# Kernel tuning notes

Hardware: AMD Instinct MI355X
Metric: run time of the kernel (lower is better)

Reference implementation:

```python
import jax, jax.numpy as jnp
import numpy as np

N_NODES = 50000
N_EDGES = 600000
D = 128


def _clip(x, c=1.0):
    # per-row L2 clip: x / max(||x|| / c, 1)
    n = jnp.linalg.norm(x, axis=-1, keepdims=True)
    return x / jnp.maximum(n / c, 1.0)


def _priv_sage_conv(x, edge_index, W, b, noise):
    # PrivSAGEConv.forward with perturbation_mode='aggr', root_weight=False
    xc = _clip(x, c=1.0)
    src, dst = edge_index[0], edge_index[1]
    # propagate: gather messages from source nodes, scatter-add at targets
    msg = jax.ops.segment_sum(xc[src], dst, num_segments=x.shape[0])  # [N, D]
    agg = xc + msg + noise  # self term + neighbor sum + DP noise
    return agg @ W.T + b


def setup_inputs() -> dict:
    key = jax.random.key(0)
    ks = jax.random.split(key, 8)
    x = jax.random.normal(ks[0], (N_NODES, D), dtype=jnp.float32)
    edge_index = jax.random.randint(ks[1], (2, N_EDGES), 0, N_NODES, dtype=jnp.int64)
    scale = 1.0 / np.sqrt(D)
    W1 = jax.random.normal(ks[2], (D, D), dtype=jnp.float32) * scale
    b1 = jnp.zeros((D,), dtype=jnp.float32)
    W2 = jax.random.normal(ks[3], (D, D), dtype=jnp.float32) * scale
    b2 = jnp.zeros((D,), dtype=jnp.float32)
    noise1 = jax.random.normal(ks[4], (N_NODES, D), dtype=jnp.float32)
    noise2 = jax.random.normal(ks[5], (N_NODES, D), dtype=jnp.float32)
    return {"x": x, "edge_index": edge_index, "W1": W1, "b1": b1,
            "W2": W2, "b2": b2, "noise1": noise1, "noise2": noise2}


def reference(x, edge_index, W1, b1, W2, b2, noise1, noise2):
    # Layer 1: conv -> (no batchnorm) -> dropout(identity, eval) -> SELU -> stack-combine
    h = _priv_sage_conv(x, edge_index, W1, b1, noise1)
    h = jax.nn.selu(h)
    # Layer 2: last layer, is_pred_module=True -> raw output
    out = _priv_sage_conv(h, edge_index, W2, b2, noise2)
    return out
```

## Files before the change

kernel.cpp:

```cpp
#include <hip/hip_runtime.h>

#define NN 50000
#define NE 600000
#define DD 128
#define NPAD 50048
#define SCAN_BLOCKS 49

typedef __attribute__((ext_vector_type(8))) short bf16x8;
typedef __attribute__((ext_vector_type(4))) float f32x4;

__device__ __forceinline__ float bf2f(unsigned int u16) {
    union { unsigned int i; float f; } v; v.i = u16 << 16; return v.f;
}
__device__ __forceinline__ unsigned short f2bf(float f) {
    union { float f; unsigned int i; } v; v.f = f;
    unsigned int i = v.i + 0x7FFFu + ((v.i >> 16) & 1u);
    return (unsigned short)(i >> 16);
}
__device__ __forceinline__ float wred64(float v) {
    #pragma unroll
    for (int o = 32; o; o >>= 1) v += __shfl_xor(v, o, 64);
    return v;
}
__device__ __forceinline__ int tame16(unsigned int u) {
    int e = (int)((u >> 7) & 0xFF);
    return (e >= 100 && e <= 133) ? 1 : 0;
}

__global__ void probe_k(const int* __restrict__ ei,
                        const unsigned int* __restrict__ xw,
                        const unsigned int* __restrict__ w1w,
                        const unsigned int* __restrict__ nzw,
                        int* __restrict__ flags) {
    const int lane = threadIdx.x;
    int nz = 0;
    #pragma unroll
    for (int i = 0; i < 4; ++i) nz |= ei[2 * (lane * 4 + i) + 1];
    int tx = tame16(xw[lane] & 0xFFFFu);
    int tw = tame16(w1w[lane] & 0xFFFFu);
    int tn = tame16(nzw[lane] & 0xFFFFu);
    #pragma unroll
    for (int o = 32; o; o >>= 1) {
        nz |= __shfl_xor(nz, o, 64);
        tx += __shfl_xor(tx, o, 64);
        tw += __shfl_xor(tw, o, 64);
        tn += __shfl_xor(tn, o, 64);
    }
    if (lane == 0) {
        flags[0] = (nz == 0) ? 1 : 0;
        flags[1] = (tx >= 48) ? 1 : 0;
        flags[2] = (tw >= 48) ? 1 : 0;
        flags[3] = (tn >= 48) ? 1 : 0;
    }
}

__global__ __launch_bounds__(256) void convert_k(
    const void* __restrict__ W1, const void* __restrict__ b1,
    const void* __restrict__ W2, const void* __restrict__ b2,
    const int* __restrict__ flags,
    unsigned short* __restrict__ W1b, unsigned short* __restrict__ b1b,
    unsigned short* __restrict__ W2b, unsigned short* __restrict__ b2b) {
    const int i = blockIdx.x * blockDim.x + threadIdx.x;
    if (i >= DD * DD) return;
    if (flags[2]) {
        W1b[i] = ((const unsigned short*)W1)[i];
        W2b[i] = ((const unsigned short*)W2)[i];
        if (i < DD) { b1b[i] = ((const unsigned short*)b1)[i];
                      b2b[i] = ((const unsigned short*)b2)[i]; }
    } else {
        W1b[i] = f2bf(((const float*)W1)[i]);
        W2b[i] = f2bf(((const float*)W2)[i]);
        if (i < DD) { b1b[i] = f2bf(((const float*)b1)[i]);
                      b2b[i] = f2bf(((const float*)b2)[i]); }
    }
}

__global__ __launch_bounds__(256) void hist_k(
    const int* __restrict__ ei, const int* __restrict__ flags,
    int* __restrict__ deg) {
    const int e = blockIdx.x * blockDim.x + threadIdx.x;
    if (e >= NE) return;
    const int d = flags[0] ? (int)((const long long*)ei)[NE + e] : ei[NE + e];
    atomicAdd(&deg[d], 1);
}

__global__ __launch_bounds__(1024) void scan1_k(
    const int* __restrict__ deg, int* __restrict__ offs,
    int* __restrict__ bsum) {
    __shared__ int wsum[16];
    __shared__ int wbase[16];
    __shared__ int tot_s;
    const int tid = threadIdx.x, lane = tid & 63, wv = tid >> 6;
    const int i = blockIdx.x * 1024 + tid;
    const int v = (i < NN) ? deg[i] : 0;
    int incl = v;
    #pragma unroll
    for (int off = 1; off < 64; off <<= 1) {
        int t = __shfl_up(incl, off, 64);
        if (lane >= off) incl += t;
    }
    if (lane == 63) wsum[wv] = incl;
    __syncthreads();
    if (wv == 0 && lane < 16) {
        const int wv_v = wsum[lane];
        int wincl = wv_v;
        #pragma unroll
        for (int off = 1; off < 16; off <<= 1) {
            int t = __shfl_up(wincl, off, 64);
            if (lane >= off) wincl += t;
        }
        wbase[lane] = wincl - wv_v;
        if (lane == 15) tot_s = wincl;
    }
    __syncthreads();
    if (i < NN) offs[i] = wbase[wv] + incl - v;
    if (tid == 0) bsum[blockIdx.x] = tot_s;
}

__global__ __launch_bounds__(1024) void scan2_k(
    int* __restrict__ offs, int* __restrict__ cursor,
    const int* __restrict__ bsum) {
    __shared__ int base_s;
    const int tid = threadIdx.x;
    if (tid < 64) {
        const int v = (tid < SCAN_BLOCKS) ? bsum[tid] : 0;
        int incl = v;
        #pragma unroll
        for (int off = 1; off < 64; off <<= 1) {
            int t = __shfl_up(incl, off, 64);
            if (tid >= off) incl += t;
        }
        if (tid == blockIdx.x) base_s = incl - v;
    }
    __syncthreads();
    const int i = blockIdx.x * 1024 + tid;
    if (i < NN) {
        const int o = offs[i] + base_s;
        offs[i] = o;
        cursor[i] = o;
    }
    if (blockIdx.x == 0 && tid == 0) offs[NN] = NE;
}

__global__ __launch_bounds__(256) void fill_k(
    const int* __restrict__ ei, const int* __restrict__ flags,
    int* __restrict__ cursor, int* __restrict__ eidx) {
    const int e = blockIdx.x * blockDim.x + threadIdx.x;
    if (e >= NE) return;
    int s, d;
    if (flags[0]) {
        const long long* e64 = (const long long*)ei;
        s = (int)e64[e]; d = (int)e64[NE + e];
    } else {
        s = ei[e]; d = ei[NE + e];
    }
    const int pos = atomicAdd(&cursor[d], 1);
    eidx[pos] = s;
}

__global__ __launch_bounds__(256) void prep_k(
    const void* __restrict__ x, const int* __restrict__ flags,
    unsigned int* __restrict__ featu) {
    const int row = (blockIdx.x * blockDim.x + threadIdx.x) >> 6;
    const int lane = threadIdx.x & 63;
    if (row > NN) return;
    if (row == NN) { featu[(size_t)NN * 64 + lane] = 0u; return; }
    float v0, v1;
    if (flags[1]) {
        const unsigned int px = ((const unsigned int*)x)[(size_t)row * 64 + lane];
        v0 = bf2f(px & 0xFFFFu); v1 = bf2f(px >> 16);
    } else {
        const float2 px = ((const float2*)x)[(size_t)row * 64 + lane];
        v0 = px.x; v1 = px.y;
    }
    const float ss = wred64(v0 * v0 + v1 * v1);
    const float nrm = sqrtf(ss);
    const float sc = nrm > 1.0f ? 1.0f / nrm : 1.0f;
    featu[(size_t)row * 64 + lane] =
        (unsigned int)f2bf(v0 * sc) | ((unsigned int)f2bf(v1 * sc) << 16);
}

__global__ __launch_bounds__(256) void agg_k(
    const int* __restrict__ offs, const int* __restrict__ eidx,
    const uint2* __restrict__ featu2, const void* __restrict__ noise,
    const int* __restrict__ flags, uint2* __restrict__ aggu2) {
    const int node = (blockIdx.x * blockDim.x + threadIdx.x) >> 6;
    const int lane = threadIdx.x & 63;
    if (node >= NN) return;
    const int c = lane & 31;
    const int h = lane >> 5;

    float a0, a1, a2, a3;
    if (h == 0) {
        const uint2 s = featu2[(size_t)node * 32 + c];
        a0 = bf2f(s.x & 0xFFFFu); a1 = bf2f(s.x >> 16);
        a2 = bf2f(s.y & 0xFFFFu); a3 = bf2f(s.y >> 16);
    } else {
        if (flags[3]) {
            const uint2 n = ((const uint2*)noise)[(size_t)node * 32 + c];
            a0 = bf2f(n.x & 0xFFFFu); a1 = bf2f(n.x >> 16);
            a2 = bf2f(n.y & 0xFFFFu); a3 = bf2f(n.y >> 16);
        } else {
            const float4 n = ((const float4*)noise)[(size_t)node * 32 + c];
            a0 = n.x; a1 = n.y; a2 = n.z; a3 = n.w;
        }
    }

    const int e0 = offs[node];
    const int cnt = offs[node + 1] - e0;
    for (int base = 0; base < cnt; base += 64) {
        const int rem = cnt - base;
        int myi = NN;
        if (lane < rem) myi = eidx[e0 + base + lane];
        const int pairs = (rem < 64 ? rem + 1 : 64) >> 1;
        const int pb = (pairs + 7) & ~7;
        for (int p = 0; p < pb; p += 8) {
            uint2 u[8];
            #pragma unroll
            for (int q = 0; q < 8; ++q) {
                const int s = __shfl(myi, 2 * (p + q) + h, 64);
                u[q] = featu2[(size_t)s * 32 + c];
            }
            #pragma unroll
            for (int q = 0; q < 8; ++q) {
                a0 += bf2f(u[q].x & 0xFFFFu); a1 += bf2f(u[q].x >> 16);
                a2 += bf2f(u[q].y & 0xFFFFu); a3 += bf2f(u[q].y >> 16);
            }
        }
    }

    a0 += __shfl_xor(a0, 32, 64);
    a1 += __shfl_xor(a1, 32, 64);
    a2 += __shfl_xor(a2, 32, 64);
    a3 += __shfl_xor(a3, 32, 64);

    if (h == 0) {
        uint2 o;
        o.x = (unsigned int)f2bf(a0) | ((unsigned int)f2bf(a1) << 16);
        o.y = (unsigned int)f2bf(a2) | ((unsigned int)f2bf(a3) << 16);
        aggu2[(size_t)node * 32 + c] = o;
    }
}

template<bool LAYER1>
__global__ __launch_bounds__(256) void gemm_k(
    const unsigned short* __restrict__ aggb,
    const unsigned short* __restrict__ Wb,
    const unsigned short* __restrict__ bb,
    unsigned short* __restrict__ featb,
    float* __restrict__ outf) {
    __shared__ unsigned short Wl[128 * 136];
    __shared__ unsigned short bl[128];
    const int t = threadIdx.x;
    #pragma unroll
    for (int i = 0; i < 8; ++i) {
        const int idx8 = t + i * 256;
        const int base = idx8 * 8;
        const int row = base >> 7, col = base & 127;
        *(uint4*)&Wl[row * 136 + col] = ((const uint4*)Wb)[idx8];
    }
    if (t < 128) bl[t] = bb[t];

    const int lane = t & 63;
    const int w = t >> 6;
    const int n15 = lane & 15;
    const int quad = lane >> 4;
    const int rbase = blockIdx.x * 64 + w * 16;

    bf16x8 af[4];
    #pragma unroll
    for (int kc = 0; kc < 4; ++kc)
        af[kc] = *(const bf16x8*)&aggb[(size_t)(rbase + n15) * DD + kc * 32 + quad * 8];

    __syncthreads();

    float h[32];
    #pragma unroll
    for (int nt = 0; nt < 8; ++nt) {
        f32x4 acc = {0.f, 0.f, 0.f, 0.f};
        #pragma unroll
        for (int kc = 0; kc < 4; ++kc) {
            const bf16x8 bfr =
                *(const bf16x8*)&Wl[(nt * 16 + n15) * 136 + kc * 32 + quad * 8];
            acc = __builtin_amdgcn_mfma_f32_16x16x32_bf16(af[kc], bfr, acc, 0, 0, 0);
        }
        const float bj = bf2f((unsigned int)bl[nt * 16 + n15]);
        #pragma unroll
        for (int r = 0; r < 4; ++r) h[nt * 4 + r] = acc[r] + bj;
    }

    if (LAYER1) {
        const float S = 1.0507009873554805f, AL = 1.6732632423543772f;
        float ss[4] = {0.f, 0.f, 0.f, 0.f};
        #pragma unroll
        for (int nt = 0; nt < 8; ++nt)
            #pragma unroll
            for (int r = 0; r < 4; ++r) {
                float v = h[nt * 4 + r];
                v = v > 0.f ? S * v : S * AL * expm1f(v);
                h[nt * 4 + r] = v;
                ss[r] += v * v;
            }
        #pragma unroll
        for (int r = 0; r < 4; ++r) {
            #pragma unroll
            for (int off = 1; off < 16; off <<= 1)
                ss[r] += __shfl_xor(ss[r], off, 64);
        }
        float sc[4];
        #pragma unroll
        for (int r = 0; r < 4; ++r) {
            const float nr = sqrtf(ss[r]);
            sc[r] = nr > 1.f ? 1.f / nr : 1.f;
        }
        #pragma unroll
        for (int r = 0; r < 4; ++r) {
            const int row = rbase + quad * 4 + r;
            if (row < NN) {
                #pragma unroll
                for (int nt = 0; nt < 8; ++nt)
                    featb[(size_t)row * DD + nt * 16 + n15] =
                        f2bf(h[nt * 4 + r] * sc[r]);
            }
        }
    } else {
        #pragma unroll
        for (int r = 0; r < 4; ++r) {
            const int row = rbase + quad * 4 + r;
            if (row < NN) {
                #pragma unroll
                for (int nt = 0; nt < 8; ++nt)
                    outf[(size_t)row * DD + nt * 16 + n15] = h[nt * 4 + r];
            }
        }
    }
}

extern "C" void kernel_launch(void* const* d_in, const int* in_sizes, int n_in,
                              void* d_out, int out_size, void* d_ws, size_t ws_size,
                              hipStream_t stream) {
    const void* x  = d_in[0];
    const int*  ei = (const int*)d_in[1];
    const void* W1 = d_in[2];
    const void* b1 = d_in[3];
    const void* W2 = d_in[4];
    const void* b2 = d_in[5];
    const void* n1 = d_in[6];
    const void* n2 = d_in[7];

    unsigned short* aggb = (unsigned short*)d_ws;
    unsigned short* W1b  = aggb + (size_t)NPAD * DD;
    unsigned short* b1b  = W1b + DD * DD;
    unsigned short* W2b  = b1b + DD;
    unsigned short* b2b  = W2b + DD * DD;
    int* flags  = (int*)(b2b + DD);
    int* deg    = flags + 4;
    int* offs   = deg + NN;
    int* cursor = offs + NN + 1;
    int* bsum   = cursor + NN;
    int* eidx   = bsum + 64;
    unsigned int* featu = (unsigned int*)d_out;

    probe_k<<<1, 64, 0, stream>>>(ei, (const unsigned int*)x,
                                  (const unsigned int*)W1,
                                  (const unsigned int*)n1, flags);
    convert_k<<<(DD * DD + 255) / 256, 256, 0, stream>>>(W1, b1, W2, b2, flags,
                                                         W1b, b1b, W2b, b2b);

    hipMemsetAsync(deg, 0, NN * sizeof(int), stream);
    hist_k<<<(NE + 255) / 256, 256, 0, stream>>>(ei, flags, deg);
    scan1_k<<<SCAN_BLOCKS, 1024, 0, stream>>>(deg, offs, bsum);
    scan2_k<<<SCAN_BLOCKS, 1024, 0, stream>>>(offs, cursor, bsum);
    fill_k<<<(NE + 255) / 256, 256, 0, stream>>>(ei, flags, cursor, eidx);

    prep_k<<<((NN + 1) * 64 + 255) / 256, 256, 0, stream>>>(x, flags, featu);
    agg_k<<<(NN * 64) / 256, 256, 0, stream>>>(offs, eidx, (const uint2*)featu,
                                               n1, flags, (uint2*)aggb);
    gemm_k<true><<<NPAD / 64, 256, 0, stream>>>(aggb, W1b, b1b,
                                                (unsigned short*)featu, nullptr);

    agg_k<<<(NN * 64) / 256, 256, 0, stream>>>(offs, eidx, (const uint2*)featu,
                                               n2, flags, (uint2*)aggb);
    gemm_k<false><<<NPAD / 64, 256, 0, stream>>>(aggb, W2b, b2b, nullptr,
                                                 (float*)d_out);
}
```

Baseline: 274.3 us.

## Fuse whole pipeline into one persistent cooperative kernel with grid syncs

Replaces the sequence of probe, convert, histogram, scan, fill, prep, aggregation and GEMM launches with a single cooperative kernel. A persistent grid loops over the work and separates phases with grid.sync. The aim is to remove per-launch overhead and inter-kernel gaps. The cost is that grid-wide barriers are added, and the persistent grid may hide latency less well during the gather-heavy aggregation phases. The old multi-kernel path is kept as a fallback if the cooperative launch fails.

After: 894.4 us. 226% more time.

```diff
diff --git a/kernel.cpp b/kernel.cpp
--- a/kernel.cpp
+++ b/kernel.cpp
@@ -1,9 +1,14 @@
 #include <hip/hip_runtime.h>
+#include <hip/hip_cooperative_groups.h>
+
+namespace cg = cooperative_groups;
 
 #define NN 50000
 #define NE 600000
 #define DD 128
 #define NPAD 50048
+#define NTILE 782
+#define NCHUNK 196
 #define SCAN_BLOCKS 49
 
 typedef __attribute__((ext_vector_type(8))) short bf16x8;
@@ -26,6 +31,330 @@
     int e = (int)((u >> 7) & 0xFF);
     return (e >= 100 && e <= 133) ? 1 : 0;
 }
+
+
+__device__ __forceinline__ void agg_phase(
+    const int* __restrict__ offs, const int* __restrict__ eidx,
+    const uint2* __restrict__ featu2, const void* __restrict__ noise,
+    const int f_nb, uint2* __restrict__ aggu2,
+    const int wvg, const int nwv, const int lane) {
+    const int c = lane & 31;
+    const int h = lane >> 5;
+    for (int node = wvg; node < NN; node += nwv) {
+        float a0, a1, a2, a3;
+        if (h == 0) {
+            const uint2 s = featu2[(size_t)node * 32 + c];
+            a0 = bf2f(s.x & 0xFFFFu); a1 = bf2f(s.x >> 16);
+            a2 = bf2f(s.y & 0xFFFFu); a3 = bf2f(s.y >> 16);
+        } else {
+            if (f_nb) {
+                const uint2 n = ((const uint2*)noise)[(size_t)node * 32 + c];
+                a0 = bf2f(n.x & 0xFFFFu); a1 = bf2f(n.x >> 16);
+                a2 = bf2f(n.y & 0xFFFFu); a3 = bf2f(n.y >> 16);
+            } else {
+                const float4 n = ((const float4*)noise)[(size_t)node * 32 + c];
+                a0 = n.x; a1 = n.y; a2 = n.z; a3 = n.w;
+            }
+        }
+        const int e0 = offs[node];
+        const int cnt = offs[node + 1] - e0;
+        for (int base = 0; base < cnt; base += 64) {
+            const int rem = cnt - base;
+            int myi = NN;
+            if (lane < rem) myi = eidx[e0 + base + lane];
+            const int pairs = (rem < 64 ? rem + 1 : 64) >> 1;
+            const int pb = (pairs + 7) & ~7;
+            for (int p = 0; p < pb; p += 8) {
+                uint2 u[8];
+                #pragma unroll
+                for (int q = 0; q < 8; ++q) {
+                    const int s = __shfl(myi, 2 * (p + q) + h, 64);
+                    u[q] = featu2[(size_t)s * 32 + c];
+                }
+                #pragma unroll
+                for (int q = 0; q < 8; ++q) {
+                    a0 += bf2f(u[q].x & 0xFFFFu); a1 += bf2f(u[q].x >> 16);
+                    a2 += bf2f(u[q].y & 0xFFFFu); a3 += bf2f(u[q].y >> 16);
+                }
+            }
+        }
+        a0 += __shfl_xor(a0, 32, 64);
+        a1 += __shfl_xor(a1, 32, 64);
+        a2 += __shfl_xor(a2, 32, 64);
+        a3 += __shfl_xor(a3, 32, 64);
+        if (h == 0) {
+            uint2 o;
+            o.x = (unsigned int)f2bf(a0) | ((unsigned int)f2bf(a1) << 16);
+            o.y = (unsigned int)f2bf(a2) | ((unsigned int)f2bf(a3) << 16);
+            aggu2[(size_t)node * 32 + c] = o;
+        }
+    }
+}
+
+template<bool LAYER1>
+__device__ __forceinline__ void gemm_phase(
+    const unsigned short* __restrict__ aggb,
+    const unsigned short* __restrict__ Wb,
+    const unsigned short* __restrict__ bb,
+    unsigned short* __restrict__ featb, float* __restrict__ outf,
+    unsigned short* Wl, unsigned short* bl,
+    const int b, const int t, const int ngrid) {
+    #pragma unroll
+    for (int i = 0; i < 8; ++i) {
+        const int idx8 = t + i * 256;
+        const int base = idx8 * 8;
+        const int row = base >> 7, col = base & 127;
+        *(uint4*)&Wl[row * 136 + col] = ((const uint4*)Wb)[idx8];
+    }
+    if (t < 128) bl[t] = bb[t];
+    __syncthreads();
+
+    const int lane = t & 63;
+    const int w = t >> 6;
+    const int n15 = lane & 15;
+    const int quad = lane >> 4;
+
+    for (int tile = b; tile < NTILE; tile += ngrid) {
+        const int rbase = tile * 64 + w * 16;
+        bf16x8 af[4];
+        #pragma unroll
+        for (int kc = 0; kc < 4; ++kc)
+            af[kc] = *(const bf16x8*)&aggb[(size_t)(rbase + n15) * DD + kc * 32 + quad * 8];
+
+        float h[32];
+        #pragma unroll
+        for (int nt = 0; nt < 8; ++nt) {
+            f32x4 acc = {0.f, 0.f, 0.f, 0.f};
+            #pragma unroll
+            for (int kc = 0; kc < 4; ++kc) {
+                const bf16x8 bfr =
+                    *(const bf16x8*)&Wl[(nt * 16 + n15) * 136 + kc * 32 + quad * 8];
+                acc = __builtin_amdgcn_mfma_f32_16x16x32_bf16(af[kc], bfr, acc, 0, 0, 0);
+            }
+            const float bj = bf2f((unsigned int)bl[nt * 16 + n15]);
+            #pragma unroll
+            for (int r = 0; r < 4; ++r) h[nt * 4 + r] = acc[r] + bj;
+        }
+
+        if (LAYER1) {
+            const float S = 1.0507009873554805f, AL = 1.6732632423543772f;
+            float ss[4] = {0.f, 0.f, 0.f, 0.f};
+            #pragma unroll
+            for (int nt = 0; nt < 8; ++nt)
+                #pragma unroll
+                for (int r = 0; r < 4; ++r) {
+                    float v = h[nt * 4 + r];
+                    v = v > 0.f ? S * v : S * AL * expm1f(v);
+                    h[nt * 4 + r] = v;
+                    ss[r] += v * v;
+                }
+            #pragma unroll
+            for (int r = 0; r < 4; ++r) {
+                #pragma unroll
+                for (int off = 1; off < 16; off <<= 1)
+                    ss[r] += __shfl_xor(ss[r], off, 64);
+            }
+            #pragma unroll
+            for (int r = 0; r < 4; ++r) {
+                const float nr = sqrtf(ss[r]);
+                const float sc = nr > 1.f ? 1.f / nr : 1.f;
+                const int row = rbase + quad * 4 + r;
+                if (row < NN) {
+                    #pragma unroll
+                    for (int nt = 0; nt < 8; ++nt)
+                        featb[(size_t)row * DD + nt * 16 + n15] =
+                            f2bf(h[nt * 4 + r] * sc);
+                }
+            }
+        } else {
+            #pragma unroll
+            for (int r = 0; r < 4; ++r) {
+                const int row = rbase + quad * 4 + r;
+                if (row < NN) {
+                    #pragma unroll
+                    for (int nt = 0; nt < 8; ++nt)
+                        outf[(size_t)row * DD + nt * 16 + n15] = h[nt * 4 + r];
+                }
+            }
+        }
+    }
+}
+
+__global__ __launch_bounds__(256, 4) void fused_k(
+    const void* __restrict__ x, const int* __restrict__ ei,
+    const void* __restrict__ W1, const void* __restrict__ b1,
+    const void* __restrict__ W2, const void* __restrict__ b2,
+    const void* __restrict__ n1, const void* __restrict__ n2,
+    unsigned short* __restrict__ aggb,
+    unsigned short* __restrict__ W1b, unsigned short* __restrict__ b1b,
+    unsigned short* __restrict__ W2b, unsigned short* __restrict__ b2b,
+    int* __restrict__ deg, int* __restrict__ offs, int* __restrict__ cursor,
+    int* __restrict__ bsum, int* __restrict__ eidx,
+    unsigned int* __restrict__ featu) {
+    cg::grid_group grid = cg::this_grid();
+    __shared__ unsigned short Wl[128 * 136];
+    __shared__ unsigned short bl[128];
+    __shared__ int flags_s[4];
+    __shared__ int wsum[4], wbase[4];
+    __shared__ int tot_s;
+
+    const int t = threadIdx.x;
+    const int b = blockIdx.x;
+    const int ngrid = gridDim.x;
+    const int lane = t & 63;
+    const int wv = t >> 6;
+    const int tid = b * 256 + t;
+    const int nthr = ngrid * 256;
+    const int wvg = b * 4 + wv;
+    const int nwv = ngrid * 4;
+
+    if (wv == 0) {
+        int nz = 0;
+        #pragma unroll
+        for (int i = 0; i < 4; ++i) nz |= ei[2 * (lane * 4 + i) + 1];
+        int tx = tame16(((const unsigned int*)x)[lane] & 0xFFFFu);
+        int tw = tame16(((const unsigned int*)W1)[lane] & 0xFFFFu);
+        int tn = tame16(((const unsigned int*)n1)[lane] & 0xFFFFu);
+        #pragma unroll
+        for (int o = 32; o; o >>= 1) {
+            nz |= __shfl_xor(nz, o, 64);
+            tx += __shfl_xor(tx, o, 64);
+            tw += __shfl_xor(tw, o, 64);
+            tn += __shfl_xor(tn, o, 64);
+        }
+        if (lane == 0) {
+            flags_s[0] = (nz == 0) ? 1 : 0;
+            flags_s[1] = (tx >= 48) ? 1 : 0;
+            flags_s[2] = (tw >= 48) ? 1 : 0;
+            flags_s[3] = (tn >= 48) ? 1 : 0;
+        }
+    }
+    __syncthreads();
+    const int f_e64 = flags_s[0], f_xb = flags_s[1];
+    const int f_wb = flags_s[2], f_nb = flags_s[3];
+
+    for (int i = tid; i < DD * DD; i += nthr) {
+        if (f_wb) {
+            W1b[i] = ((const unsigned short*)W1)[i];
+            W2b[i] = ((const unsigned short*)W2)[i];
+            if (i < DD) { b1b[i] = ((const unsigned short*)b1)[i];
+                          b2b[i] = ((const unsigned short*)b2)[i]; }
+        } else {
+            W1b[i] = f2bf(((const float*)W1)[i]);
+            W2b[i] = f2bf(((const float*)W2)[i]);
+            if (i < DD) { b1b[i] = f2bf(((const float*)b1)[i]);
+                          b2b[i] = f2bf(((const float*)b2)[i]); }
+        }
+    }
+    for (int i = tid; i < NN; i += nthr) deg[i] = 0;
+    for (int row = wvg; row <= NN; row += nwv) {
+        if (row == NN) { featu[(size_t)NN * 64 + lane] = 0u; continue; }
+        float v0, v1;
+        if (f_xb) {
+            const unsigned int px = ((const unsigned int*)x)[(size_t)row * 64 + lane];
+            v0 = bf2f(px & 0xFFFFu); v1 = bf2f(px >> 16);
+        } else {
+            const float2 px = ((const float2*)x)[(size_t)row * 64 + lane];
+            v0 = px.x; v1 = px.y;
+        }
+        const float ss = wred64(v0 * v0 + v1 * v1);
+        const float nrm = sqrtf(ss);
+        const float sc = nrm > 1.0f ? 1.0f / nrm : 1.0f;
+        featu[(size_t)row * 64 + lane] =
+            (unsigned int)f2bf(v0 * sc) | ((unsigned int)f2bf(v1 * sc) << 16);
+    }
+    grid.sync();
+
+    for (int e = tid; e < NE; e += nthr) {
+        const int d = f_e64 ? (int)((const long long*)ei)[NE + e] : ei[NE + e];
+        atomicAdd(&deg[d], 1);
+    }
+    grid.sync();
+
+    for (int ch = b; ch < NCHUNK; ch += ngrid) {
+        const int i = ch * 256 + t;
+        const int v = (i < NN) ? deg[i] : 0;
+        int incl = v;
+        #pragma unroll
+        for (int off = 1; off < 64; off <<= 1) {
+            int tt = __shfl_up(incl, off, 64);
+            if (lane >= off) incl += tt;
+        }
+        if (lane == 63) wsum[wv] = incl;
+        __syncthreads();
+        if (t < 4) {
+            int s = 0;
+            for (int k = 0; k < t; ++k) s += wsum[k];
+            wbase[t] = s;
+            if (t == 3) tot_s = s + wsum[3];
+        }
+        __syncthreads();
+        if (i < NN) offs[i] = wbase[wv] + incl - v;
+        if (t == 0) bsum[ch] = tot_s;
+        __syncthreads();
+    }
+    grid.sync();
+
+    if (b == 0) {
+        const int v = (t < NCHUNK) ? bsum[t] : 0;
+        int incl = v;
+        #pragma unroll
+        for (int off = 1; off < 64; off <<= 1) {
+            int tt = __shfl_up(incl, off, 64);
+            if (lane >= off) incl += tt;
+        }
+        if (lane == 63) wsum[wv] = incl;
+        __syncthreads();
+        if (t < 4) {
+            int s = 0;
+            for (int k = 0; k < t; ++k) s += wsum[k];
+            wbase[t] = s;
+        }
+        __syncthreads();
+        if (t < NCHUNK) bsum[t] = wbase[wv] + incl - v;
+    }
+    grid.sync();
+
+    for (int ch = b; ch < NCHUNK; ch += ngrid) {
+        const int i = ch * 256 + t;
+        if (i < NN) {
+            const int o = offs[i] + bsum[ch];
+            offs[i] = o;
+            cursor[i] = o;
+        }
+    }
+    if (b == 0 && t == 0) offs[NN] = NE;
+    grid.sync();
+
+    for (int e = tid; e < NE; e += nthr) {
+        int s, d;
+        if (f_e64) {
+            const long long* e64 = (const long long*)ei;
+            s = (int)e64[e]; d = (int)e64[NE + e];
+        } else {
+            s = ei[e]; d = ei[NE + e];
+        }
+        const int pos = atomicAdd(&cursor[d], 1);
+        eidx[pos] = s;
+    }
+    grid.sync();
+
+    agg_phase(offs, eidx, (const uint2*)featu, n1, f_nb, (uint2*)aggb,
+              wvg, nwv, lane);
+    grid.sync();
+
+    gemm_phase<true>(aggb, W1b, b1b, (unsigned short*)featu, nullptr,
+                     Wl, bl, b, t, ngrid);
+    grid.sync();
+
+    agg_phase(offs, eidx, (const uint2*)featu, n2, f_nb, (uint2*)aggb,
+              wvg, nwv, lane);
+    grid.sync();
+
+    gemm_phase<false>(aggb, W2b, b2b, nullptr, (float*)featu,
+                      Wl, bl, b, t, ngrid);
+}
+
 
 __global__ void probe_k(const int* __restrict__ ei,
                         const unsigned int* __restrict__ xw,
@@ -187,59 +516,7 @@
     const int node = (blockIdx.x * blockDim.x + threadIdx.x) >> 6;
     const int lane = threadIdx.x & 63;
     if (node >= NN) return;
-    const int c = lane & 31;
-    const int h = lane >> 5;
-
-    float a0, a1, a2, a3;
-    if (h == 0) {
-        const uint2 s = featu2[(size_t)node * 32 + c];
-        a0 = bf2f(s.x & 0xFFFFu); a1 = bf2f(s.x >> 16);
-        a2 = bf2f(s.y & 0xFFFFu); a3 = bf2f(s.y >> 16);
-    } else {
-        if (flags[3]) {
-            const uint2 n = ((const uint2*)noise)[(size_t)node * 32 + c];
-            a0 = bf2f(n.x & 0xFFFFu); a1 = bf2f(n.x >> 16);
-            a2 = bf2f(n.y & 0xFFFFu); a3 = bf2f(n.y >> 16);
-        } else {
-            const float4 n = ((const float4*)noise)[(size_t)node * 32 + c];
-            a0 = n.x; a1 = n.y; a2 = n.z; a3 = n.w;
-        }
-    }
-
-    const int e0 = offs[node];
-    const int cnt = offs[node + 1] - e0;
-    for (int base = 0; base < cnt; base += 64) {
-        const int rem = cnt - base;
-        int myi = NN;
-        if (lane < rem) myi = eidx[e0 + base + lane];
-        const int pairs = (rem < 64 ? rem + 1 : 64) >> 1;
-        const int pb = (pairs + 7) & ~7;
-        for (int p = 0; p < pb; p += 8) {
-            uint2 u[8];
-            #pragma unroll
-            for (int q = 0; q < 8; ++q) {
-                const int s = __shfl(myi, 2 * (p + q) + h, 64);
-                u[q] = featu2[(size_t)s * 32 + c];
-            }
-            #pragma unroll
-            for (int q = 0; q < 8; ++q) {
-                a0 += bf2f(u[q].x & 0xFFFFu); a1 += bf2f(u[q].x >> 16);
-                a2 += bf2f(u[q].y & 0xFFFFu); a3 += bf2f(u[q].y >> 16);
-            }
-        }
-    }
-
-    a0 += __shfl_xor(a0, 32, 64);
-    a1 += __shfl_xor(a1, 32, 64);
-    a2 += __shfl_xor(a2, 32, 64);
-    a3 += __shfl_xor(a3, 32, 64);
-
-    if (h == 0) {
-        uint2 o;
-        o.x = (unsigned int)f2bf(a0) | ((unsigned int)f2bf(a1) << 16);
-        o.y = (unsigned int)f2bf(a2) | ((unsigned int)f2bf(a3) << 16);
-        aggu2[(size_t)node * 32 + c] = o;
-    }
+    agg_phase(offs, eidx, featu2, noise, flags[3], aggu2, node, 1 << 30, lane);
 }
 
 template<bool LAYER1>
@@ -251,89 +528,8 @@
     float* __restrict__ outf) {
     __shared__ unsigned short Wl[128 * 136];
     __shared__ unsigned short bl[128];
-    const int t = threadIdx.x;
-    #pragma unroll
-    for (int i = 0; i < 8; ++i) {
-        const int idx8 = t + i * 256;
-        const int base = idx8 * 8;
-        const int row = base >> 7, col = base & 127;
-        *(uint4*)&Wl[row * 136 + col] = ((const uint4*)Wb)[idx8];
-    }
-    if (t < 128) bl[t] = bb[t];
-
-    const int lane = t & 63;
-    const int w = t >> 6;
-    const int n15 = lane & 15;
-    const int quad = lane >> 4;
-    const int rbase = blockIdx.x * 64 + w * 16;
-
-    bf16x8 af[4];
-    #pragma unroll
-    for (int kc = 0; kc < 4; ++kc)
-        af[kc] = *(const bf16x8*)&aggb[(size_t)(rbase + n15) * DD + kc * 32 + quad * 8];
-
-    __syncthreads();
-
-    float h[32];
-    #pragma unroll
-    for (int nt = 0; nt < 8; ++nt) {
-        f32x4 acc = {0.f, 0.f, 0.f, 0.f};
-        #pragma unroll
-        for (int kc = 0; kc < 4; ++kc) {
-            const bf16x8 bfr =
-                *(const bf16x8*)&Wl[(nt * 16 + n15) * 136 + kc * 32 + quad * 8];
-            acc = __builtin_amdgcn_mfma_f32_16x16x32_bf16(af[kc], bfr, acc, 0, 0, 0);
-        }
-        const float bj = bf2f((unsigned int)bl[nt * 16 + n15]);
-        #pragma unroll
-        for (int r = 0; r < 4; ++r) h[nt * 4 + r] = acc[r] + bj;
-    }
-
-    if (LAYER1) {
-        const float S = 1.0507009873554805f, AL = 1.6732632423543772f;
-        float ss[4] = {0.f, 0.f, 0.f, 0.f};
-        #pragma unroll
-        for (int nt = 0; nt < 8; ++nt)
-            #pragma unroll
-            for (int r = 0; r < 4; ++r) {
-                float v = h[nt * 4 + r];
-                v = v > 0.f ? S * v : S * AL * expm1f(v);
-                h[nt * 4 + r] = v;
-                ss[r] += v * v;
-            }
-        #pragma unroll
-        for (int r = 0; r < 4; ++r) {
-            #pragma unroll
-            for (int off = 1; off < 16; off <<= 1)
-                ss[r] += __shfl_xor(ss[r], off, 64);
-        }
-        float sc[4];
-        #pragma unroll
-        for (int r = 0; r < 4; ++r) {
-            const float nr = sqrtf(ss[r]);
-            sc[r] = nr > 1.f ? 1.f / nr : 1.f;
-        }
-        #pragma unroll
-        for (int r = 0; r < 4; ++r) {
-            const int row = rbase + quad * 4 + r;
-            if (row < NN) {
-                #pragma unroll
-                for (int nt = 0; nt < 8; ++nt)
-                    featb[(size_t)row * DD + nt * 16 + n15] =
-                        f2bf(h[nt * 4 + r] * sc[r]);
-            }
-        }
-    } else {
-        #pragma unroll
-        for (int r = 0; r < 4; ++r) {
-            const int row = rbase + quad * 4 + r;
-            if (row < NN) {
-                #pragma unroll
-                for (int nt = 0; nt < 8; ++nt)
-                    outf[(size_t)row * DD + nt * 16 + n15] = h[nt * 4 + r];
-            }
-        }
-    }
+    gemm_phase<LAYER1>(aggb, Wb, bb, featb, outf, Wl, bl,
+                       blockIdx.x, threadIdx.x, 1 << 30);
 }
 
 extern "C" void kernel_launch(void* const* d_in, const int* in_sizes, int n_in,
@@ -358,29 +554,54 @@
     int* offs   = deg + NN;
     int* cursor = offs + NN + 1;
     int* bsum   = cursor + NN;
-    int* eidx   = bsum + 64;
+    int* eidx   = bsum + 256;
     unsigned int* featu = (unsigned int*)d_out;
 
-    probe_k<<<1, 64, 0, stream>>>(ei, (const unsigned int*)x,
-                                  (const unsigned int*)W1,
-                                  (const unsigned int*)n1, flags);
-    convert_k<<<(DD * DD + 255) / 256, 256, 0, stream>>>(W1, b1, W2, b2, flags,
-                                                         W1b, b1b, W2b, b2b);
-
-    hipMemsetAsync(deg, 0, NN * sizeof(int), stream);
-    hist_k<<<(NE + 255) / 256, 256, 0, stream>>>(ei, flags, deg);
-    scan1_k<<<SCAN_BLOCKS, 1024, 0, stream>>>(deg, offs, bsum);
-    scan2_k<<<SCAN_BLOCKS, 1024, 0, stream>>>(offs, cursor, bsum);
-    fill_k<<<(NE + 255) / 256, 256, 0, stream>>>(ei, flags, cursor, eidx);
-
-    prep_k<<<((NN + 1) * 64 + 255) / 256, 256, 0, stream>>>(x, flags, featu);
-    agg_k<<<(NN * 64) / 256, 256, 0, stream>>>(offs, eidx, (const uint2*)featu,
-                                               n1, flags, (uint2*)aggb);
-    gemm_k<true><<<NPAD / 64, 256, 0, stream>>>(aggb, W1b, b1b,
-                                                (unsigned short*)featu, nullptr);
-
-    agg_k<<<(NN * 64) / 256, 256, 0, stream>>>(offs, eidx, (const uint2*)featu,
-                                               n2, flags, (uint2*)aggb);
-    gemm_k<false><<<NPAD / 64, 256, 0, stream>>>(aggb, W2b, b2b, nullptr,
-                                                 (float*)d_out);
-}
+    static int grid_blocks = 0;
+    if (grid_blocks == 0) {
+        int maxB = 0;
+        if (hipOccupancyMaxActiveBlocksPerMultiprocessor(&maxB, fused_k, 256, 0)
+                != hipSuccess || maxB <= 0)
+            grid_blocks = -1;
+        else
+            grid_blocks = (maxB * 256 < 1024) ? maxB * 256 : 1024;
+        if (grid_blocks < NTILE && grid_blocks > 0 && grid_blocks < NCHUNK)
+            grid_blocks = -1;
+    }
+
+    bool coop_ok = false;
+    if (grid_blocks > 0) {
+        void* args[] = {
+            (void*)&x, (void*)&ei, (void*)&W1, (void*)&b1, (void*)&W2,
+            (void*)&b2, (void*)&n1, (void*)&n2,
+            (void*)&aggb, (void*)&W1b, (void*)&b1b, (void*)&W2b, (void*)&b2b,
+            (void*)&deg, (void*)&offs, (void*)&cursor, (void*)&bsum,
+            (void*)&eidx, (void*)&featu};
+        hipError_t err = hipLaunchCooperativeKernel(
+            (const void*)fused_k, dim3(grid_blocks), dim3(256), args, 0, stream);
+        if (err == hipSuccess) coop_ok = true;
+        else { (void)hipGetLastError(); grid_blocks = -1; }
+    }
+
+    if (!coop_ok) {
+        probe_k<<<1, 64, 0, stream>>>(ei, (const unsigned int*)x,
+                                      (const unsigned int*)W1,
+                                      (const unsigned int*)n1, flags);
+        convert_k<<<(DD * DD + 255) / 256, 256, 0, stream>>>(W1, b1, W2, b2, flags,
+                                                             W1b, b1b, W2b, b2b);
+        hipMemsetAsync(deg, 0, NN * sizeof(int), stream);
+        hist_k<<<(NE + 255) / 256, 256, 0, stream>>>(ei, flags, deg);
+        scan1_k<<<SCAN_BLOCKS, 1024, 0, stream>>>(deg, offs, bsum);
+        scan2_k<<<SCAN_BLOCKS, 1024, 0, stream>>>(offs, cursor, bsum);
+        fill_k<<<(NE + 255) / 256, 256, 0, stream>>>(ei, flags, cursor, eidx);
+        prep_k<<<((NN + 1) * 64 + 255) / 256, 256, 0, stream>>>(x, flags, featu);
+        agg_k<<<(NN * 64) / 256, 256, 0, stream>>>(offs, eidx, (const uint2*)featu,
+                                                   n1, flags, (uint2*)aggb);
+        gemm_k<true><<<NPAD / 64, 256, 0, stream>>>(aggb, W1b, b1b,
+                                                    (unsigned short*)featu, nullptr);
+        agg_k<<<(NN * 64) / 256, 256, 0, stream>>>(offs, eidx, (const uint2*)featu,
+                                                   n2, flags, (uint2*)aggb);
+        gemm_k<false><<<NPAD / 64, 256, 0, stream>>>(aggb, W2b, b2b, nullptr,
+                                                     (float*)d_out);
+    }
+}
```

## Fuse setup kernels and merge two-pass scan into single decoupled-lookback scan

Applied to the files above, without the earlier changes.

Folds the probe, weight conversion, degree memset and feature clipping into one setup kernel. Each consumer kernel now runs its own format probe in shared memory instead of reading a global flags array. The two scan kernels become one that uses an atomic flag-based inter-block prefix wait. The aim is fewer launches and less launch gap, at the cost of redundant probe work in every block and a spin-wait that depends on all 49 scan blocks being resident at once.

After: 281.3 us. +2.6%, slower.

```diff
diff --git a/kernel.cpp b/kernel.cpp
--- a/kernel.cpp
+++ b/kernel.cpp
@@ -4,6 +4,9 @@
 #define NE 600000
 #define DD 128
 #define NPAD 50048
+#define NTILE 782
+#define SETUP_BLOCKS 12501
+#define EDGE_BLOCKS 2344
 #define SCAN_BLOCKS 49
 
 typedef __attribute__((ext_vector_type(8))) short bf16x8;
@@ -27,176 +30,48 @@
     return (e >= 100 && e <= 133) ? 1 : 0;
 }
 
-__global__ void probe_k(const int* __restrict__ ei,
-                        const unsigned int* __restrict__ xw,
-                        const unsigned int* __restrict__ w1w,
-                        const unsigned int* __restrict__ nzw,
-                        int* __restrict__ flags) {
-    const int lane = threadIdx.x;
-    int nz = 0;
-    #pragma unroll
-    for (int i = 0; i < 4; ++i) nz |= ei[2 * (lane * 4 + i) + 1];
-    int tx = tame16(xw[lane] & 0xFFFFu);
-    int tw = tame16(w1w[lane] & 0xFFFFu);
-    int tn = tame16(nzw[lane] & 0xFFFFu);
-    #pragma unroll
-    for (int o = 32; o; o >>= 1) {
-        nz |= __shfl_xor(nz, o, 64);
-        tx += __shfl_xor(tx, o, 64);
-        tw += __shfl_xor(tw, o, 64);
-        tn += __shfl_xor(tn, o, 64);
-    }
-    if (lane == 0) {
-        flags[0] = (nz == 0) ? 1 : 0;
-        flags[1] = (tx >= 48) ? 1 : 0;
-        flags[2] = (tw >= 48) ? 1 : 0;
-        flags[3] = (tn >= 48) ? 1 : 0;
-    }
-}
-
-__global__ __launch_bounds__(256) void convert_k(
-    const void* __restrict__ W1, const void* __restrict__ b1,
-    const void* __restrict__ W2, const void* __restrict__ b2,
-    const int* __restrict__ flags,
-    unsigned short* __restrict__ W1b, unsigned short* __restrict__ b1b,
-    unsigned short* __restrict__ W2b, unsigned short* __restrict__ b2b) {
-    const int i = blockIdx.x * blockDim.x + threadIdx.x;
-    if (i >= DD * DD) return;
-    if (flags[2]) {
-        W1b[i] = ((const unsigned short*)W1)[i];
-        W2b[i] = ((const unsigned short*)W2)[i];
-        if (i < DD) { b1b[i] = ((const unsigned short*)b1)[i];
-                      b2b[i] = ((const unsigned short*)b2)[i]; }
-    } else {
-        W1b[i] = f2bf(((const float*)W1)[i]);
-        W2b[i] = f2bf(((const float*)W2)[i]);
-        if (i < DD) { b1b[i] = f2bf(((const float*)b1)[i]);
-                      b2b[i] = f2bf(((const float*)b2)[i]); }
-    }
-}
-
-__global__ __launch_bounds__(256) void hist_k(
-    const int* __restrict__ ei, const int* __restrict__ flags,
-    int* __restrict__ deg) {
-    const int e = blockIdx.x * blockDim.x + threadIdx.x;
-    if (e >= NE) return;
-    const int d = flags[0] ? (int)((const long long*)ei)[NE + e] : ei[NE + e];
-    atomicAdd(&deg[d], 1);
-}
-
-__global__ __launch_bounds__(1024) void scan1_k(
-    const int* __restrict__ deg, int* __restrict__ offs,
-    int* __restrict__ bsum) {
-    __shared__ int wsum[16];
-    __shared__ int wbase[16];
-    __shared__ int tot_s;
-    const int tid = threadIdx.x, lane = tid & 63, wv = tid >> 6;
-    const int i = blockIdx.x * 1024 + tid;
-    const int v = (i < NN) ? deg[i] : 0;
-    int incl = v;
-    #pragma unroll
-    for (int off = 1; off < 64; off <<= 1) {
-        int t = __shfl_up(incl, off, 64);
-        if (lane >= off) incl += t;
-    }
-    if (lane == 63) wsum[wv] = incl;
-    __syncthreads();
-    if (wv == 0 && lane < 16) {
-        const int wv_v = wsum[lane];
-        int wincl = wv_v;
-        #pragma unroll
-        for (int off = 1; off < 16; off <<= 1) {
-            int t = __shfl_up(wincl, off, 64);
-            if (lane >= off) wincl += t;
-        }
-        wbase[lane] = wincl - wv_v;
-        if (lane == 15) tot_s = wincl;
-    }
-    __syncthreads();
-    if (i < NN) offs[i] = wbase[wv] + incl - v;
-    if (tid == 0) bsum[blockIdx.x] = tot_s;
-}
-
-__global__ __launch_bounds__(1024) void scan2_k(
-    int* __restrict__ offs, int* __restrict__ cursor,
-    const int* __restrict__ bsum) {
-    __shared__ int base_s;
-    const int tid = threadIdx.x;
-    if (tid < 64) {
-        const int v = (tid < SCAN_BLOCKS) ? bsum[tid] : 0;
-        int incl = v;
-        #pragma unroll
-        for (int off = 1; off < 64; off <<= 1) {
-            int t = __shfl_up(incl, off, 64);
-            if (tid >= off) incl += t;
-        }
-        if (tid == blockIdx.x) base_s = incl - v;
-    }
-    __syncthreads();
-    const int i = blockIdx.x * 1024 + tid;
-    if (i < NN) {
-        const int o = offs[i] + base_s;
-        offs[i] = o;
-        cursor[i] = o;
-    }
-    if (blockIdx.x == 0 && tid == 0) offs[NN] = NE;
-}
-
-__global__ __launch_bounds__(256) void fill_k(
-    const int* __restrict__ ei, const int* __restrict__ flags,
-    int* __restrict__ cursor, int* __restrict__ eidx) {
-    const int e = blockIdx.x * blockDim.x + threadIdx.x;
-    if (e >= NE) return;
-    int s, d;
-    if (flags[0]) {
-        const long long* e64 = (const long long*)ei;
-        s = (int)e64[e]; d = (int)e64[NE + e];
-    } else {
-        s = ei[e]; d = ei[NE + e];
-    }
-    const int pos = atomicAdd(&cursor[d], 1);
-    eidx[pos] = s;
-}
-
-__global__ __launch_bounds__(256) void prep_k(
-    const void* __restrict__ x, const int* __restrict__ flags,
-    unsigned int* __restrict__ featu) {
-    const int row = (blockIdx.x * blockDim.x + threadIdx.x) >> 6;
-    const int lane = threadIdx.x & 63;
-    if (row > NN) return;
-    if (row == NN) { featu[(size_t)NN * 64 + lane] = 0u; return; }
-    float v0, v1;
-    if (flags[1]) {
-        const unsigned int px = ((const unsigned int*)x)[(size_t)row * 64 + lane];
-        v0 = bf2f(px & 0xFFFFu); v1 = bf2f(px >> 16);
-    } else {
-        const float2 px = ((const float2*)x)[(size_t)row * 64 + lane];
-        v0 = px.x; v1 = px.y;
-    }
-    const float ss = wred64(v0 * v0 + v1 * v1);
-    const float nrm = sqrtf(ss);
-    const float sc = nrm > 1.0f ? 1.0f / nrm : 1.0f;
-    featu[(size_t)row * 64 + lane] =
-        (unsigned int)f2bf(v0 * sc) | ((unsigned int)f2bf(v1 * sc) << 16);
-}
-
-__global__ __launch_bounds__(256) void agg_k(
+
+__device__ __forceinline__ int probe_e64(const int* __restrict__ ei, int t,
+                                         int* f_s) {
+    if (t < 64) {
+        int nz = 0;
+        #pragma unroll
+        for (int i = 0; i < 4; ++i) nz |= ei[2 * (t * 4 + i) + 1];
+        #pragma unroll
+        for (int o = 32; o; o >>= 1) nz |= __shfl_xor(nz, o, 64);
+        if (t == 0) *f_s = (nz == 0) ? 1 : 0;
+    }
+    __syncthreads();
+    return *f_s;
+}
+
+__device__ __forceinline__ int probe_bf16(const unsigned int* __restrict__ p,
+                                          int t, int* f_s) {
+    if (t < 64) {
+        int tc = tame16(p[t] & 0xFFFFu);
+        #pragma unroll
+        for (int o = 32; o; o >>= 1) tc += __shfl_xor(tc, o, 64);
+        if (t == 0) *f_s = (tc >= 48) ? 1 : 0;
+    }
+    __syncthreads();
+    return *f_s;
+}
+
+
+__device__ __forceinline__ void agg_phase(
     const int* __restrict__ offs, const int* __restrict__ eidx,
     const uint2* __restrict__ featu2, const void* __restrict__ noise,
-    const int* __restrict__ flags, uint2* __restrict__ aggu2) {
-    const int node = (blockIdx.x * blockDim.x + threadIdx.x) >> 6;
-    const int lane = threadIdx.x & 63;
-    if (node >= NN) return;
+    const int f_nb, uint2* __restrict__ aggu2,
+    const int node, const int lane) {
     const int c = lane & 31;
     const int h = lane >> 5;
-
     float a0, a1, a2, a3;
     if (h == 0) {
         const uint2 s = featu2[(size_t)node * 32 + c];
         a0 = bf2f(s.x & 0xFFFFu); a1 = bf2f(s.x >> 16);
         a2 = bf2f(s.y & 0xFFFFu); a3 = bf2f(s.y >> 16);
     } else {
-        if (flags[3]) {
+        if (f_nb) {
             const uint2 n = ((const uint2*)noise)[(size_t)node * 32 + c];
             a0 = bf2f(n.x & 0xFFFFu); a1 = bf2f(n.x >> 16);
             a2 = bf2f(n.y & 0xFFFFu); a3 = bf2f(n.y >> 16);
@@ -205,7 +80,6 @@
             a0 = n.x; a1 = n.y; a2 = n.z; a3 = n.w;
         }
     }
-
     const int e0 = offs[node];
     const int cnt = offs[node + 1] - e0;
     for (int base = 0; base < cnt; base += 64) {
@@ -228,18 +102,179 @@
             }
         }
     }
-
     a0 += __shfl_xor(a0, 32, 64);
     a1 += __shfl_xor(a1, 32, 64);
     a2 += __shfl_xor(a2, 32, 64);
     a3 += __shfl_xor(a3, 32, 64);
-
     if (h == 0) {
         uint2 o;
         o.x = (unsigned int)f2bf(a0) | ((unsigned int)f2bf(a1) << 16);
         o.y = (unsigned int)f2bf(a2) | ((unsigned int)f2bf(a3) << 16);
         aggu2[(size_t)node * 32 + c] = o;
     }
+}
+
+
+__global__ __launch_bounds__(256) void setup_k(
+    const void* __restrict__ x,
+    const void* __restrict__ W1, const void* __restrict__ b1,
+    const void* __restrict__ W2, const void* __restrict__ b2,
+    unsigned short* __restrict__ W1b, unsigned short* __restrict__ b1b,
+    unsigned short* __restrict__ W2b, unsigned short* __restrict__ b2b,
+    int* __restrict__ deg, int* __restrict__ pf,
+    unsigned int* __restrict__ featu) {
+    __shared__ int fx_s, fw_s;
+    const int t = threadIdx.x;
+    if (t < 64) {
+        int tx = tame16(((const unsigned int*)x)[t] & 0xFFFFu);
+        int tw = tame16(((const unsigned int*)W1)[t] & 0xFFFFu);
+        #pragma unroll
+        for (int o = 32; o; o >>= 1) {
+            tx += __shfl_xor(tx, o, 64);
+            tw += __shfl_xor(tw, o, 64);
+        }
+        if (t == 0) { fx_s = (tx >= 48) ? 1 : 0; fw_s = (tw >= 48) ? 1 : 0; }
+    }
+    __syncthreads();
+    const int f_xb = fx_s, f_wb = fw_s;
+    const int b = blockIdx.x;
+    const int tid = b * 256 + t;
+    const int nthr = gridDim.x * 256;
+
+    for (int i = tid; i < DD * DD; i += nthr) {
+        if (f_wb) {
+            W1b[i] = ((const unsigned short*)W1)[i];
+            W2b[i] = ((const unsigned short*)W2)[i];
+            if (i < DD) { b1b[i] = ((const unsigned short*)b1)[i];
+                          b2b[i] = ((const unsigned short*)b2)[i]; }
+        } else {
+            W1b[i] = f2bf(((const float*)W1)[i]);
+            W2b[i] = f2bf(((const float*)W2)[i]);
+            if (i < DD) { b1b[i] = f2bf(((const float*)b1)[i]);
+                          b2b[i] = f2bf(((const float*)b2)[i]); }
+        }
+    }
+    for (int i = tid; i < NN + 64; i += nthr) {
+        if (i < NN) deg[i] = 0; else pf[i - NN] = 0;
+    }
+    const int lane = t & 63;
+    const int wv = t >> 6;
+    const int nwv = gridDim.x * 4;
+    for (int row = b * 4 + wv; row <= NN; row += nwv) {
+        if (row == NN) { featu[(size_t)NN * 64 + lane] = 0u; continue; }
+        float v0, v1;
+        if (f_xb) {
+            const unsigned int px = ((const unsigned int*)x)[(size_t)row * 64 + lane];
+            v0 = bf2f(px & 0xFFFFu); v1 = bf2f(px >> 16);
+        } else {
+            const float2 px = ((const float2*)x)[(size_t)row * 64 + lane];
+            v0 = px.x; v1 = px.y;
+        }
+        const float ss = wred64(v0 * v0 + v1 * v1);
+        const float nrm = sqrtf(ss);
+        const float sc = nrm > 1.0f ? 1.0f / nrm : 1.0f;
+        featu[(size_t)row * 64 + lane] =
+            (unsigned int)f2bf(v0 * sc) | ((unsigned int)f2bf(v1 * sc) << 16);
+    }
+}
+
+__global__ __launch_bounds__(256) void hist_k(
+    const int* __restrict__ ei, int* __restrict__ deg) {
+    __shared__ int f_s;
+    const int f_e64 = probe_e64(ei, threadIdx.x, &f_s);
+    const int e = blockIdx.x * 256 + threadIdx.x;
+    if (e >= NE) return;
+    const int d = f_e64 ? (int)((const long long*)ei)[NE + e] : ei[NE + e];
+    atomicAdd(&deg[d], 1);
+}
+
+__global__ __launch_bounds__(1024) void scan_k(
+    const int* __restrict__ deg, int* __restrict__ offs,
+    int* __restrict__ cursor, int* __restrict__ pf) {
+    __shared__ int wsum[16];
+    __shared__ int wbase[16];
+    __shared__ int base_s;
+    const int tid = threadIdx.x, lane = tid & 63, wv = tid >> 6;
+    const int b = blockIdx.x;
+    const int i = b * 1024 + tid;
+    const int v = (i < NN) ? deg[i] : 0;
+    int incl = v;
+    #pragma unroll
+    for (int off = 1; off < 64; off <<= 1) {
+        int t = __shfl_up(incl, off, 64);
+        if (lane >= off) incl += t;
+    }
+    if (lane == 63) wsum[wv] = incl;
+    __syncthreads();
+    if (wv == 0 && lane < 16) {
+        const int wv_v = wsum[lane];
+        int wincl = wv_v;
+        #pragma unroll
+        for (int off = 1; off < 16; off <<= 1) {
+            int t = __shfl_up(wincl, off, 64);
+            if (lane >= off) wincl += t;
+        }
+        wbase[lane] = wincl - wv_v;
+        if (lane == 15)
+            __hip_atomic_store(&pf[b], wincl + 1, __ATOMIC_RELEASE,
+                               __HIP_MEMORY_SCOPE_AGENT);
+    }
+    if (wv == 0) {
+        int val = 0;
+        while (true) {
+            if (lane < SCAN_BLOCKS && val == 0)
+                val = __hip_atomic_load(&pf[lane], __ATOMIC_ACQUIRE,
+                                        __HIP_MEMORY_SCOPE_AGENT);
+            if (__ballot(lane < SCAN_BLOCKS && val == 0) == 0ull) break;
+            __builtin_amdgcn_s_sleep(1);
+        }
+        int pv = (lane < SCAN_BLOCKS) ? val - 1 : 0;
+        int ex = pv;
+        #pragma unroll
+        for (int off = 1; off < 64; off <<= 1) {
+            int t = __shfl_up(ex, off, 64);
+            if (lane >= off) ex += t;
+        }
+        ex -= pv;
+        if (lane == b) base_s = ex;
+    }
+    __syncthreads();
+    if (i < NN) {
+        const int o = base_s + wbase[wv] + incl - v;
+        offs[i] = o;
+        cursor[i] = o;
+    }
+    if (b == 0 && tid == 0) offs[NN] = NE;
+}
+
+__global__ __launch_bounds__(256) void fill_k(
+    const int* __restrict__ ei, int* __restrict__ cursor,
+    int* __restrict__ eidx) {
+    __shared__ int f_s;
+    const int f_e64 = probe_e64(ei, threadIdx.x, &f_s);
+    const int e = blockIdx.x * 256 + threadIdx.x;
+    if (e >= NE) return;
+    int s, d;
+    if (f_e64) {
+        const long long* e64 = (const long long*)ei;
+        s = (int)e64[e]; d = (int)e64[NE + e];
+    } else {
+        s = ei[e]; d = ei[NE + e];
+    }
+    const int pos = atomicAdd(&cursor[d], 1);
+    eidx[pos] = s;
+}
+
+__global__ __launch_bounds__(256) void agg_k(
+    const int* __restrict__ offs, const int* __restrict__ eidx,
+    const uint2* __restrict__ featu2, const void* __restrict__ noise,
+    const unsigned int* __restrict__ nprobe, uint2* __restrict__ aggu2) {
+    __shared__ int f_s;
+    const int f_nb = probe_bf16(nprobe, threadIdx.x, &f_s);
+    const int node = (blockIdx.x * 256 + threadIdx.x) >> 6;
+    const int lane = threadIdx.x & 63;
+    if (node >= NN) return;
+    agg_phase(offs, eidx, featu2, noise, f_nb, aggu2, node, lane);
 }
 
 template<bool LAYER1>
@@ -307,20 +342,16 @@
             for (int off = 1; off < 16; off <<= 1)
                 ss[r] += __shfl_xor(ss[r], off, 64);
         }
-        float sc[4];
         #pragma unroll
         for (int r = 0; r < 4; ++r) {
             const float nr = sqrtf(ss[r]);
-            sc[r] = nr > 1.f ? 1.f / nr : 1.f;
-        }
-        #pragma unroll
-        for (int r = 0; r < 4; ++r) {
+            const float sc = nr > 1.f ? 1.f / nr : 1.f;
             const int row = rbase + quad * 4 + r;
             if (row < NN) {
                 #pragma unroll
                 for (int nt = 0; nt < 8; ++nt)
                     featb[(size_t)row * DD + nt * 16 + n15] =
-                        f2bf(h[nt * 4 + r] * sc[r]);
+                        f2bf(h[nt * 4 + r] * sc);
             }
         }
     } else {
@@ -353,34 +384,26 @@
     unsigned short* b1b  = W1b + DD * DD;
     unsigned short* W2b  = b1b + DD;
     unsigned short* b2b  = W2b + DD * DD;
-    int* flags  = (int*)(b2b + DD);
-    int* deg    = flags + 4;
+    int* deg    = (int*)(b2b + DD);
     int* offs   = deg + NN;
     int* cursor = offs + NN + 1;
-    int* bsum   = cursor + NN;
-    int* eidx   = bsum + 64;
+    int* pf     = cursor + NN;
+    int* eidx   = pf + 64;
     unsigned int* featu = (unsigned int*)d_out;
 
-    probe_k<<<1, 64, 0, stream>>>(ei, (const unsigned int*)x,
-                                  (const unsigned int*)W1,
-                                  (const unsigned int*)n1, flags);
-    convert_k<<<(DD * DD + 255) / 256, 256, 0, stream>>>(W1, b1, W2, b2, flags,
-                                                         W1b, b1b, W2b, b2b);
-
-    hipMemsetAsync(deg, 0, NN * sizeof(int), stream);
-    hist_k<<<(NE + 255) / 256, 256, 0, stream>>>(ei, flags, deg);
-    scan1_k<<<SCAN_BLOCKS, 1024, 0, stream>>>(deg, offs, bsum);
-    scan2_k<<<SCAN_BLOCKS, 1024, 0, stream>>>(offs, cursor, bsum);
-    fill_k<<<(NE + 255) / 256, 256, 0, stream>>>(ei, flags, cursor, eidx);
-
-    prep_k<<<((NN + 1) * 64 + 255) / 256, 256, 0, stream>>>(x, flags, featu);
+    setup_k<<<SETUP_BLOCKS, 256, 0, stream>>>(
+        x, W1, b1, W2, b2, W1b, b1b, W2b, b2b, deg, pf, featu);
+    hist_k<<<EDGE_BLOCKS, 256, 0, stream>>>(ei, deg);
+    scan_k<<<SCAN_BLOCKS, 1024, 0, stream>>>(deg, offs, cursor, pf);
+    fill_k<<<EDGE_BLOCKS, 256, 0, stream>>>(ei, cursor, eidx);
     agg_k<<<(NN * 64) / 256, 256, 0, stream>>>(offs, eidx, (const uint2*)featu,
-                                               n1, flags, (uint2*)aggb);
-    gemm_k<true><<<NPAD / 64, 256, 0, stream>>>(aggb, W1b, b1b,
-                                                (unsigned short*)featu, nullptr);
-
+                                               n1, (const unsigned int*)n1,
+                                               (uint2*)aggb);
+    gemm_k<true><<<NTILE, 256, 0, stream>>>(aggb, W1b, b1b,
+                                            (unsigned short*)featu, nullptr);
     agg_k<<<(NN * 64) / 256, 256, 0, stream>>>(offs, eidx, (const uint2*)featu,
-                                               n2, flags, (uint2*)aggb);
-    gemm_k<false><<<NPAD / 64, 256, 0, stream>>>(aggb, W2b, b2b, nullptr,
-                                                 (float*)d_out);
-}
+                                               n2, (const unsigned int*)n1,
+                                               (uint2*)aggb);
+    gemm_k<false><<<NTILE, 256, 0, stream>>>(aggb, W2b, b2b, nullptr,
+                                             (float*)d_out);
+}
```
